# Performance work log

Hardware: AMD Instinct MI355X
Metric: run time of the kernel (lower is better)

The kernel has to match this reference:

```python
import jax, jax.numpy as jnp
import numpy as np

BETA = 0.25
NUM_SEMANTIC = 8192
EPS = 1e-8  # torch F.normalize / cosine_similarity eps


def _normalize(v, axis=-1):
    n = jnp.linalg.norm(v, axis=axis, keepdims=True)
    return v / jnp.maximum(n, EPS)


def _cos_sim(a, b):
    # faithful to F.cosine_similarity(a, b, dim=-1)
    na = jnp.maximum(jnp.linalg.norm(a, axis=-1), EPS)
    nb = jnp.maximum(jnp.linalg.norm(b, axis=-1), EPS)
    return jnp.sum(a * b, axis=-1) / (na * nb)


def setup_inputs() -> dict:
    key = jax.random.key(0)
    k1, k2, k3 = jax.random.split(key, 3)
    x = jax.random.normal(k1, (8192, 1024), dtype=jnp.float32)
    semantic_embeddings = jax.random.normal(k2, (8192, 1024), dtype=jnp.float32)
    # trunc_normal_(std=0.02) ~ clipped normal; plain scaled normal is a fine init stand-in
    learnable_entries = 0.02 * jax.random.normal(k3, (128, 1024), dtype=jnp.float32)
    return {"x": x, "semantic_embeddings": semantic_embeddings,
            "learnable_entries": learnable_entries}


def reference(x, semantic_embeddings, learnable_entries):
    frozen = _normalize(semantic_embeddings)          # [S, D] (buffer, pre-normalized)
    learned = _normalize(learnable_entries)           # [L, D]
    codebook = jnp.concatenate([frozen, learned], 0)  # [S+L, D]

    xn = _normalize(x)                                # [N, D]
    logits = xn @ codebook.T                          # [N, S+L]
    indices = jnp.argmax(logits, axis=-1)             # [N]
    z_q = codebook[indices]                           # [N, D]
    z_q_st = xn + jax.lax.stop_gradient(z_q - xn)

    is_learnable = (indices >= NUM_SEMANTIC).astype(jnp.float32)
    commitment_loss = jnp.mean(1.0 - _cos_sim(xn, jax.lax.stop_gradient(z_q)))
    per_token = 1.0 - _cos_sim(jax.lax.stop_gradient(xn), z_q)
    vq_loss = jnp.sum(per_token * is_learnable) / (jnp.sum(is_learnable) + 1e-6)
    quant_loss = vq_loss + BETA * commitment_loss

    return logits, indices, z_q, z_q_st, vq_loss, commitment_loss, quant_loss
```

## Files before the change

### kernel.cpp

```cpp
#include <hip/hip_runtime.h>
#include <stdint.h>


#define N_TOK   8192
#define DIM     1024
#define N_SEM   8192
#define N_LEARN 128
#define N_CODE  (N_SEM + N_LEARN)

typedef _Float16 f16;
typedef _Float16 f16x4 __attribute__((ext_vector_type(4)));
typedef _Float16 f16x8 __attribute__((ext_vector_type(8)));
typedef float    f32x4 __attribute__((ext_vector_type(4)));

__global__ void k_init(unsigned long long* keys) {
    int i = blockIdx.x * blockDim.x + threadIdx.x;
    if (i < N_TOK) keys[i] = 0ULL;
}

__global__ __launch_bounds__(256) void k_norm_split(
    const float* __restrict__ in, float* __restrict__ invn,
    f16* __restrict__ hi, f16* __restrict__ lo)
{
    const int row = blockIdx.x;
    const int t = threadIdx.x;
    float4 v = ((const float4*)(in + (size_t)row * DIM))[t];
    float ss = v.x*v.x + v.y*v.y + v.z*v.z + v.w*v.w;
    #pragma unroll
    for (int off = 32; off > 0; off >>= 1) ss += __shfl_xor(ss, off);
    __shared__ float red[4];
    if ((t & 63) == 0) red[t >> 6] = ss;

    f16 h0 = (f16)v.x, h1 = (f16)v.y, h2 = (f16)v.z, h3 = (f16)v.w;
    f16x4 hv = {h0, h1, h2, h3};
    f16x4 lv = {(f16)(v.x - (float)h0), (f16)(v.y - (float)h1),
                (f16)(v.z - (float)h2), (f16)(v.w - (float)h3)};
    ((f16x4*)(hi + (size_t)row * DIM))[t] = hv;
    ((f16x4*)(lo + (size_t)row * DIM))[t] = lv;

    __syncthreads();
    if (t == 0) {
        float tot = red[0] + red[1] + red[2] + red[3];
        invn[row] = 1.f / fmaxf(sqrtf(tot), 1e-8f);
    }
}

#define BM 128
#define BN 128
#define BK 32

__device__ __forceinline__ void gload16(const void* g, void* l) {
    __builtin_amdgcn_global_load_lds(
        (const __attribute__((address_space(1))) void*)g,
        (__attribute__((address_space(3))) void*)l, 16, 0, 0);
}

__global__ __launch_bounds__(256) void k_gemm_mfma(
    const f16* __restrict__ xHi,  const f16* __restrict__ xLo,
    const f16* __restrict__ semHi, const f16* __restrict__ semLo,
    const f16* __restrict__ lrnHi, const f16* __restrict__ lrnLo,
    const float* __restrict__ invnx, const float* __restrict__ invnb,
    float* __restrict__ logits, unsigned long long* __restrict__ keys)
{
    __shared__ __align__(16) f16 sAh[BM * BK];
    __shared__ __align__(16) f16 sAl[BM * BK];
    __shared__ __align__(16) f16 sBh[BN * BK];
    __shared__ __align__(16) f16 sBl[BN * BK];

    const int t    = threadIdx.x;
    const int lane = t & 63;
    const int wid  = t >> 6;
    const int row0 = blockIdx.x * BM;
    const int col0 = blockIdx.y * BN;
    const int wm   = (wid >> 1) * 64;
    const int wn   = (wid & 1) * 64;

    const f16* bh; const f16* bl;
    if (col0 < N_SEM) { bh = semHi + (size_t)col0 * DIM;
                        bl = semLo + (size_t)col0 * DIM; }
    else              { bh = lrnHi + (size_t)(col0 - N_SEM) * DIM;
                        bl = lrnLo + (size_t)(col0 - N_SEM) * DIM; }
    const f16* ah = xHi + (size_t)row0 * DIM;
    const f16* al = xLo + (size_t)row0 * DIM;

    const int sr = t >> 2;
    const int sc = (t & 3) ^ ((sr >> 1) & 3);
    const size_t g0 = (size_t)sr * DIM + sc * 8;
    const size_t g1 = g0 + (size_t)64 * DIM;
    f16* lA0  = sAh + t * 8;  f16* lA1  = sAh + t * 8 + 2048;
    f16* lAl0 = sAl + t * 8;  f16* lAl1 = sAl + t * 8 + 2048;
    f16* lB0  = sBh + t * 8;  f16* lB1  = sBh + t * 8 + 2048;
    f16* lBl0 = sBl + t * 8;  f16* lBl1 = sBl + t * 8 + 2048;

    f32x4 acc[4][4];
    #pragma unroll
    for (int i = 0; i < 4; ++i)
        #pragma unroll
        for (int j = 0; j < 4; ++j) acc[i][j] = (f32x4)0.f;

    const int fr  = lane & 15;
    const int fg  = lane >> 4;
    const int swz = fg ^ ((fr >> 1) & 3);
    const f16* rAh = sAh + (wm + fr) * BK + swz * 8;
    const f16* rAl = sAl + (wm + fr) * BK + swz * 8;
    const f16* rBh = sBh + (wn + fr) * BK + swz * 8;
    const f16* rBl = sBl + (wn + fr) * BK + swz * 8;

    #pragma unroll 1
    for (int k0 = 0; k0 < DIM; k0 += BK) {
        gload16(ah + g0 + k0, lA0);
        gload16(ah + g1 + k0, lA1);
        gload16(al + g0 + k0, lAl0);
        gload16(al + g1 + k0, lAl1);
        gload16(bh + g0 + k0, lB0);
        gload16(bh + g1 + k0, lB1);
        gload16(bl + g0 + k0, lBl0);
        gload16(bl + g1 + k0, lBl1);
        __syncthreads();

        f16x8 aH[4], aL[4], bH[4], bL[4];
        #pragma unroll
        for (int f = 0; f < 4; ++f) {
            aH[f] = *(const f16x8*)(rAh + f * 16 * BK);
            aL[f] = *(const f16x8*)(rAl + f * 16 * BK);
            bH[f] = *(const f16x8*)(rBh + f * 16 * BK);
            bL[f] = *(const f16x8*)(rBl + f * 16 * BK);
        }
        #pragma unroll
        for (int i = 0; i < 4; ++i)
            #pragma unroll
            for (int j = 0; j < 4; ++j) {
                acc[i][j] = __builtin_amdgcn_mfma_f32_16x16x32_f16(aH[i], bH[j], acc[i][j], 0, 0, 0);
                acc[i][j] = __builtin_amdgcn_mfma_f32_16x16x32_f16(aH[i], bL[j], acc[i][j], 0, 0, 0);
                acc[i][j] = __builtin_amdgcn_mfma_f32_16x16x32_f16(aL[i], bH[j], acc[i][j], 0, 0, 0);
            }
        __syncthreads();
    }

    float ibv[4];
    #pragma unroll
    for (int fn = 0; fn < 4; ++fn) ibv[fn] = invnb[col0 + wn + fn * 16 + fr];

    #pragma unroll
    for (int fm = 0; fm < 4; ++fm) {
        #pragma unroll
        for (int reg = 0; reg < 4; ++reg) {
            const int row = row0 + wm + fm * 16 + fg * 4 + reg;
            const float ia = invnx[row];
            float best = -3.4e38f; int bcol = 0;
            float* dst = logits + (size_t)row * N_CODE + col0 + wn + fr;
            #pragma unroll
            for (int fn = 0; fn < 4; ++fn) {
                float v = acc[fm][fn][reg] * (ia * ibv[fn]);
                dst[fn * 16] = v;
                int c = col0 + wn + fn * 16 + fr;
                if (v > best) { best = v; bcol = c; }
            }
            #pragma unroll
            for (int off = 8; off > 0; off >>= 1) {
                float ov = __shfl_xor(best, off);
                int   oc = __shfl_xor(bcol, off);
                if (ov > best || (ov == best && oc < bcol)) { best = ov; bcol = oc; }
            }
            if (fr == 0) {
                unsigned int u = __float_as_uint(best);
                unsigned int s = (u & 0x80000000u) ? ~u : (u | 0x80000000u);
                unsigned long long key = ((unsigned long long)s << 14) |
                                         (unsigned long long)(16383 - bcol);
                atomicMax(keys + row, key);
            }
        }
    }
}

__global__ __launch_bounds__(256) void k_epilogue(
    const float* __restrict__ X,
    const float* __restrict__ SEM,
    const float* __restrict__ LRN,
    const float* __restrict__ invnx,
    const float* __restrict__ invnb,
    const unsigned long long* __restrict__ keys,
    float* __restrict__ o_idx,
    float* __restrict__ o_zq,
    float* __restrict__ o_zst,
    float* __restrict__ perTok)
{
    const int tok = blockIdx.x;
    const int t = threadIdx.x;
    const int col = 16383 - (int)(keys[tok] & 16383ULL);
    const float ix = invnx[tok];
    const float ib = invnb[col];
    const float* crow = (col < N_SEM) ? (SEM + (size_t)col * DIM)
                                      : (LRN + (size_t)(col - N_SEM) * DIM);

    float4 xr = ((const float4*)(X + (size_t)tok * DIM))[t];
    float4 cr = ((const float4*)crow)[t];
    float4 xv; xv.x = xr.x*ix; xv.y = xr.y*ix; xv.z = xr.z*ix; xv.w = xr.w*ix;
    float4 zv; zv.x = cr.x*ib; zv.y = cr.y*ib; zv.z = cr.z*ib; zv.w = cr.w*ib;

    float d  = xv.x*zv.x + xv.y*zv.y + xv.z*zv.z + xv.w*zv.w;
    float nx = xv.x*xv.x + xv.y*xv.y + xv.z*xv.z + xv.w*xv.w;
    float nz = zv.x*zv.x + zv.y*zv.y + zv.z*zv.z + zv.w*zv.w;
    #pragma unroll
    for (int off = 32; off > 0; off >>= 1) {
        d  += __shfl_xor(d, off);
        nx += __shfl_xor(nx, off);
        nz += __shfl_xor(nz, off);
    }
    __shared__ float rd[4], rx[4], rz[4];
    if ((t & 63) == 0) { rd[t>>6] = d; rx[t>>6] = nx; rz[t>>6] = nz; }
    __syncthreads();

    float4 zs;
    zs.x = xv.x + (zv.x - xv.x);
    zs.y = xv.y + (zv.y - xv.y);
    zs.z = xv.z + (zv.z - xv.z);
    zs.w = xv.w + (zv.w - xv.w);
    ((float4*)o_zq)[(size_t)tok * 256 + t] = zv;
    ((float4*)o_zst)[(size_t)tok * 256 + t] = zs;

    if (t == 0) {
        float D  = rd[0]+rd[1]+rd[2]+rd[3];
        float NX = rx[0]+rx[1]+rx[2]+rx[3];
        float NZ = rz[0]+rz[1]+rz[2]+rz[3];
        float cs = D / (fmaxf(sqrtf(NX), 1e-8f) * fmaxf(sqrtf(NZ), 1e-8f));
        o_idx[tok]  = (float)col;
        perTok[tok] = 1.f - cs;
    }
}

__global__ __launch_bounds__(256) void k_final(
    const float* __restrict__ perTok,
    const float* __restrict__ o_idx,
    float* __restrict__ o_scal)
{
    const int t = threadIdx.x;
    float cs = 0.f, vs = 0.f, vc = 0.f;
    for (int i = t; i < N_TOK; i += 256) {
        float p = perTok[i];
        cs += p;
        if (o_idx[i] >= (float)N_SEM) { vs += p; vc += 1.f; }
    }
    #pragma unroll
    for (int off = 32; off > 0; off >>= 1) {
        cs += __shfl_xor(cs, off);
        vs += __shfl_xor(vs, off);
        vc += __shfl_xor(vc, off);
    }
    __shared__ float r0[4], r1[4], r2[4];
    if ((t & 63) == 0) { r0[t>>6] = cs; r1[t>>6] = vs; r2[t>>6] = vc; }
    __syncthreads();
    if (t == 0) {
        float C = r0[0]+r0[1]+r0[2]+r0[3];
        float V = r1[0]+r1[1]+r1[2]+r1[3];
        float K = r2[0]+r2[1]+r2[2]+r2[3];
        float commit = C / (float)N_TOK;
        float vq     = V / (K + 1e-6f);
        o_scal[0] = vq;
        o_scal[1] = commit;
        o_scal[2] = vq + 0.25f * commit;
    }
}

extern "C" void kernel_launch(void* const* d_in, const int* in_sizes, int n_in,
                              void* d_out, int out_size, void* d_ws, size_t ws_size,
                              hipStream_t stream) {
    const float* x   = (const float*)d_in[0];
    const float* sem = (const float*)d_in[1];
    const float* lrn = (const float*)d_in[2];

    float* invnx = (float*)d_ws;
    float* invnb = invnx + N_TOK;
    unsigned long long* keys = (unsigned long long*)(invnb + N_CODE);
    float* perTok = (float*)(keys + N_TOK);
    f16* lrnHi = (f16*)(perTok + N_TOK);
    f16* lrnLo = lrnHi + (size_t)N_LEARN * DIM;

    float* out      = (float*)d_out;
    float* o_logits = out;
    float* o_idx    = o_logits + (size_t)N_TOK * N_CODE;
    float* o_zq     = o_idx + N_TOK;
    float* o_zst    = o_zq + (size_t)N_TOK * DIM;
    float* o_scal   = o_zst + (size_t)N_TOK * DIM;

    f16* xHi   = (f16*)o_zq;
    f16* xLo   = xHi + (size_t)N_TOK * DIM;
    f16* semHi = (f16*)o_zst;
    f16* semLo = semHi + (size_t)N_SEM * DIM;

    k_init<<<(N_TOK + 255) / 256, 256, 0, stream>>>(keys);
    k_norm_split<<<N_TOK,   256, 0, stream>>>(x,   invnx,         xHi,   xLo);
    k_norm_split<<<N_SEM,   256, 0, stream>>>(sem, invnb,         semHi, semLo);
    k_norm_split<<<N_LEARN, 256, 0, stream>>>(lrn, invnb + N_SEM, lrnHi, lrnLo);

    dim3 g2(N_TOK / BM, N_CODE / BN);
    k_gemm_mfma<<<g2, 256, 0, stream>>>(xHi, xLo, semHi, semLo, lrnHi, lrnLo,
                                        invnx, invnb, o_logits, keys);

    k_epilogue<<<N_TOK, 256, 0, stream>>>(x, sem, lrn, invnx, invnb, keys,
                                          o_idx, o_zq, o_zst, perTok);
    k_final<<<1, 256, 0, stream>>>(perTok, o_idx, o_scal);
}
```

Before: 884.4 us.

## Double-buffer hi tiles in LDS, load lo fragments from global, fuse prep kernels

The GEMM now double-buffers only the high-half f16 tiles in LDS. The next stage is prefetched while the current one is computed, so there is one barrier per K step instead of two. The low-half correction fragments are read straight from global memory into registers rather than staged through LDS. The init and three normalize/split launches are merged into a single prep kernel. The aim is to overlap global loads with MFMA work and cut LDS traffic and launch overhead, at the cost of uncoalesced direct global reads for the lo operands.

```diff
diff --git a/kernel.cpp b/kernel.cpp
--- a/kernel.cpp
+++ b/kernel.cpp
@@ -13,17 +13,28 @@
 typedef _Float16 f16x8 __attribute__((ext_vector_type(8)));
 typedef float    f32x4 __attribute__((ext_vector_type(4)));
 
-__global__ void k_init(unsigned long long* keys) {
-    int i = blockIdx.x * blockDim.x + threadIdx.x;
-    if (i < N_TOK) keys[i] = 0ULL;
-}
-
-__global__ __launch_bounds__(256) void k_norm_split(
-    const float* __restrict__ in, float* __restrict__ invn,
-    f16* __restrict__ hi, f16* __restrict__ lo)
+__global__ __launch_bounds__(256) void k_prep(
+    const float* __restrict__ x,   float* __restrict__ invnx,
+    f16* __restrict__ xHi,  f16* __restrict__ xLo,
+    const float* __restrict__ sem, float* __restrict__ invnb,
+    f16* __restrict__ semHi, f16* __restrict__ semLo,
+    const float* __restrict__ lrn,
+    f16* __restrict__ lrnHi, f16* __restrict__ lrnLo,
+    unsigned long long* __restrict__ keys)
 {
-    const int row = blockIdx.x;
+    const int b = blockIdx.x;
     const int t = threadIdx.x;
+    const float* in; float* invn; f16* hi; f16* lo; int row;
+    if (b < N_TOK) {
+        row = b; in = x; invn = invnx; hi = xHi; lo = xLo;
+        if (t == 0) keys[row] = 0ULL;
+    } else if (b < N_TOK + N_SEM) {
+        row = b - N_TOK; in = sem; invn = invnb; hi = semHi; lo = semLo;
+    } else {
+        row = b - N_TOK - N_SEM; in = lrn; invn = invnb + N_SEM;
+        hi = lrnHi; lo = lrnLo;
+    }
+
     float4 v = ((const float4*)(in + (size_t)row * DIM))[t];
     float ss = v.x*v.x + v.y*v.y + v.z*v.z + v.w*v.w;
     #pragma unroll
@@ -62,10 +73,8 @@
     const float* __restrict__ invnx, const float* __restrict__ invnb,
     float* __restrict__ logits, unsigned long long* __restrict__ keys)
 {
-    __shared__ __align__(16) f16 sAh[BM * BK];
-    __shared__ __align__(16) f16 sAl[BM * BK];
-    __shared__ __align__(16) f16 sBh[BN * BK];
-    __shared__ __align__(16) f16 sBl[BN * BK];
+    __shared__ __align__(16) f16 sA[2][BM * BK];
+    __shared__ __align__(16) f16 sB[2][BN * BK];
 
     const int t    = threadIdx.x;
     const int lane = t & 63;
@@ -75,67 +84,78 @@
     const int wm   = (wid >> 1) * 64;
     const int wn   = (wid & 1) * 64;
 
-    const f16* bh; const f16* bl;
+    const f16* bh; const f16* blo;
     if (col0 < N_SEM) { bh = semHi + (size_t)col0 * DIM;
-                        bl = semLo + (size_t)col0 * DIM; }
+                        blo = semLo + (size_t)col0 * DIM; }
     else              { bh = lrnHi + (size_t)(col0 - N_SEM) * DIM;
-                        bl = lrnLo + (size_t)(col0 - N_SEM) * DIM; }
-    const f16* ah = xHi + (size_t)row0 * DIM;
-    const f16* al = xLo + (size_t)row0 * DIM;
+                        blo = lrnLo + (size_t)(col0 - N_SEM) * DIM; }
+    const f16* ah  = xHi + (size_t)row0 * DIM;
+    const f16* alo = xLo + (size_t)row0 * DIM;
 
     const int sr = t >> 2;
     const int sc = (t & 3) ^ ((sr >> 1) & 3);
     const size_t g0 = (size_t)sr * DIM + sc * 8;
     const size_t g1 = g0 + (size_t)64 * DIM;
-    f16* lA0  = sAh + t * 8;  f16* lA1  = sAh + t * 8 + 2048;
-    f16* lAl0 = sAl + t * 8;  f16* lAl1 = sAl + t * 8 + 2048;
-    f16* lB0  = sBh + t * 8;  f16* lB1  = sBh + t * 8 + 2048;
-    f16* lBl0 = sBl + t * 8;  f16* lBl1 = sBl + t * 8 + 2048;
-
-    f32x4 acc[4][4];
-    #pragma unroll
-    for (int i = 0; i < 4; ++i)
-        #pragma unroll
-        for (int j = 0; j < 4; ++j) acc[i][j] = (f32x4)0.f;
 
     const int fr  = lane & 15;
     const int fg  = lane >> 4;
     const int swz = fg ^ ((fr >> 1) & 3);
-    const f16* rAh = sAh + (wm + fr) * BK + swz * 8;
-    const f16* rAl = sAl + (wm + fr) * BK + swz * 8;
-    const f16* rBh = sBh + (wn + fr) * BK + swz * 8;
-    const f16* rBl = sBl + (wn + fr) * BK + swz * 8;
-
+
+    const f16* aLb = alo + (size_t)(wm + fr) * DIM + fg * 8;
+    const f16* bLb = blo + (size_t)(wn + fr) * DIM + fg * 8;
+
+    f32x4 acc[4][4];
+    #pragma unroll
+    for (int i = 0; i < 4; ++i)
+        #pragma unroll
+        for (int j = 0; j < 4; ++j) acc[i][j] = (f32x4)0.f;
+
+#define STAGE(b, k0) do { \
+        gload16(ah + g0 + (k0), &sA[b][t * 8]); \
+        gload16(ah + g1 + (k0), &sA[b][t * 8 + 2048]); \
+        gload16(bh + g0 + (k0), &sB[b][t * 8]); \
+        gload16(bh + g1 + (k0), &sB[b][t * 8 + 2048]); \
+    } while (0)
+
+    STAGE(0, 0);
+    asm volatile("s_waitcnt vmcnt(0)" ::: "memory");
+    __builtin_amdgcn_s_barrier();
+
+    int cur = 0;
     #pragma unroll 1
     for (int k0 = 0; k0 < DIM; k0 += BK) {
-        gload16(ah + g0 + k0, lA0);
-        gload16(ah + g1 + k0, lA1);
-        gload16(al + g0 + k0, lAl0);
-        gload16(al + g1 + k0, lAl1);
-        gload16(bh + g0 + k0, lB0);
-        gload16(bh + g1 + k0, lB1);
-        gload16(bl + g0 + k0, lBl0);
-        gload16(bl + g1 + k0, lBl1);
-        __syncthreads();
-
-        f16x8 aH[4], aL[4], bH[4], bL[4];
+        f16x8 aL[4], bL[4];
         #pragma unroll
         for (int f = 0; f < 4; ++f) {
-            aH[f] = *(const f16x8*)(rAh + f * 16 * BK);
-            aL[f] = *(const f16x8*)(rAl + f * 16 * BK);
-            bH[f] = *(const f16x8*)(rBh + f * 16 * BK);
-            bL[f] = *(const f16x8*)(rBl + f * 16 * BK);
+            aL[f] = *(const f16x8*)(aLb + (size_t)f * 16 * DIM + k0);
+            bL[f] = *(const f16x8*)(bLb + (size_t)f * 16 * DIM + k0);
         }
+        if (k0 + BK < DIM) STAGE(cur ^ 1, k0 + BK);
+
+        f16x8 aH[4], bH[4];
+        #pragma unroll
+        for (int f = 0; f < 4; ++f) {
+            aH[f] = *(const f16x8*)(&sA[cur][(wm + f * 16 + fr) * BK + swz * 8]);
+            bH[f] = *(const f16x8*)(&sB[cur][(wn + f * 16 + fr) * BK + swz * 8]);
+        }
+        #pragma unroll
+        for (int i = 0; i < 4; ++i)
+            #pragma unroll
+            for (int j = 0; j < 4; ++j)
+                acc[i][j] = __builtin_amdgcn_mfma_f32_16x16x32_f16(aH[i], bH[j], acc[i][j], 0, 0, 0);
         #pragma unroll
         for (int i = 0; i < 4; ++i)
             #pragma unroll
             for (int j = 0; j < 4; ++j) {
-                acc[i][j] = __builtin_amdgcn_mfma_f32_16x16x32_f16(aH[i], bH[j], acc[i][j], 0, 0, 0);
                 acc[i][j] = __builtin_amdgcn_mfma_f32_16x16x32_f16(aH[i], bL[j], acc[i][j], 0, 0, 0);
                 acc[i][j] = __builtin_amdgcn_mfma_f32_16x16x32_f16(aL[i], bH[j], acc[i][j], 0, 0, 0);
             }
-        __syncthreads();
-    }
+
+        asm volatile("s_waitcnt vmcnt(0)" ::: "memory");
+        __builtin_amdgcn_s_barrier();
+        cur ^= 1;
+    }
+#undef STAGE
 
     float ibv[4];
     #pragma unroll
@@ -288,10 +308,8 @@
     f16* semHi = (f16*)o_zst;
     f16* semLo = semHi + (size_t)N_SEM * DIM;
 
-    k_init<<<(N_TOK + 255) / 256, 256, 0, stream>>>(keys);
-    k_norm_split<<<N_TOK,   256, 0, stream>>>(x,   invnx,         xHi,   xLo);
-    k_norm_split<<<N_SEM,   256, 0, stream>>>(sem, invnb,         semHi, semLo);
-    k_norm_split<<<N_LEARN, 256, 0, stream>>>(lrn, invnb + N_SEM, lrnHi, lrnLo);
+    k_prep<<<N_TOK + N_SEM + N_LEARN, 256, 0, stream>>>(
+        x, invnx, xHi, xLo, sem, invnb, semHi, semLo, lrn, lrnHi, lrnLo, keys);
 
     dim3 g2(N_TOK / BM, N_CODE / BN);
     k_gemm_mfma<<<g2, 256, 0, stream>>>(xHi, xLo, semHi, semLo, lrnHi, lrnLo,
```

Measured after the change: 1.005 ms. +13.6%, slower.
